# Kernel tuning notes

Hardware: AMD Instinct MI355X
Metric: run time of the kernel (lower is better)

The kernel has to match this reference:

```python
import jax, jax.numpy as jnp
import numpy as np

N_NODES = 100_000
N_EDGES = 600_000
D = 128  # in_channels


def setup_inputs() -> dict:
    key = jax.random.key(0)
    k1, k2, k3, k4, k5 = jax.random.split(key, 5)
    node_embs_src = jax.random.normal(k1, (N_NODES, D), dtype=jnp.float32)
    node_embs_dst = jax.random.normal(k2, (N_NODES, D), dtype=jnp.float32)
    edge_index = jax.random.randint(k3, (2, N_EDGES), 0, N_NODES, dtype=jnp.int64)
    # MLP params: Linear(2D -> D), Linear(D -> 1); scaled like default torch init
    W1 = jax.random.normal(k4, (2 * D, D), dtype=jnp.float32) / np.sqrt(2 * D)
    b1 = jnp.zeros((D,), dtype=jnp.float32)
    W2 = jax.random.normal(k5, (D, 1), dtype=jnp.float32) / np.sqrt(D)
    b2 = jnp.zeros((1,), dtype=jnp.float32)
    return {
        "node_embs_src": node_embs_src,
        "node_embs_dst": node_embs_dst,
        "edge_index": edge_index,
        "W1": W1,
        "b1": b1,
        "W2": W2,
        "b2": b2,
    }


def reference(node_embs_src, node_embs_dst, edge_index, W1, b1, W2, b2):
    # Gather per-edge source / destination embeddings: [E, D] each
    src = node_embs_src[edge_index[0]]
    dst = node_embs_dst[edge_index[1]]
    # concat([src, dst]) @ W1 == src @ W1[:D] + dst @ W1[D:]  (avoids materializing [E, 2D])
    h = jnp.dot(src, W1[:D]) + jnp.dot(dst, W1[D:]) + b1  # [E, D]
    h = jax.nn.relu(h)
    logits = jnp.dot(h, W2) + b2  # [E, 1]
    return jax.nn.sigmoid(logits)
```

## Files before the change

kernel.cpp:

```cpp
#include <hip/hip_runtime.h>
#include <stdint.h>

typedef __attribute__((ext_vector_type(8))) short short8;
typedef __attribute__((ext_vector_type(4))) float f32x4;

__device__ __forceinline__ unsigned short f2bf(float f) {
  union { float f; uint32_t u; } v; v.f = f;
  uint32_t u = v.u;
  uint32_t r = (u + 0x7FFFu + ((u >> 16) & 1u)) >> 16;
  return (unsigned short)r;
}
__device__ __forceinline__ float bf2f(unsigned short h) {
  union { uint32_t u; float f; } v; v.u = ((uint32_t)h) << 16; return v.f;
}

#define NBM 64
__global__ __launch_bounds__(256, 8)
void node_phase_kernel(const float* __restrict__ src_emb,
                       const float* __restrict__ dst_emb,
                       const float* __restrict__ W1,
                       unsigned short* __restrict__ UV,
                       int Nn, int ntiles) {
  __shared__ __align__(16) char Als[NBM * 256];

  const int tbl = blockIdx.y;
  const float* emb = tbl ? dst_emb : src_emb;
  const float* Wt  = W1 + (size_t)tbl * 128 * 128;
  unsigned short* outp = UV + (size_t)tbl * Nn * 128;

  const int tid  = threadIdx.x;
  const int lane = tid & 63;
  const int w    = tid >> 6;
  const int l15  = lane & 15;
  const int lk8  = (lane >> 4) * 8;

  short8 bfrag[4][2];
#pragma unroll
  for (int s = 0; s < 4; ++s) {
#pragma unroll
    for (int nf = 0; nf < 2; ++nf) {
      const int col = w * 32 + nf * 16 + l15;
      short8 t;
#pragma unroll
      for (int j = 0; j < 8; ++j) {
        const int k = s * 32 + lk8 + j;
        t[j] = (short)f2bf(Wt[k * 128 + col]);
      }
      bfrag[s][nf] = t;
    }
  }

  const int q = tid & 15, r0 = tid >> 4;
  const int swz = (l15 & 7) << 4;

  for (int t = blockIdx.x; t < ntiles; t += gridDim.x) {
    const int t0 = t * NBM;

#pragma unroll
    for (int i = 0; i < 4; ++i) {
      const int row = i * 16 + r0;
      const int node = t0 + row;
      if (node < Nn) {
        const float* base = emb + (size_t)node * 128 + q * 8;
        const float4 f0 = *(const float4*)base;
        const float4 f1 = *(const float4*)(base + 4);
        short8 hv;
        hv[0] = (short)f2bf(f0.x); hv[1] = (short)f2bf(f0.y);
        hv[2] = (short)f2bf(f0.z); hv[3] = (short)f2bf(f0.w);
        hv[4] = (short)f2bf(f1.x); hv[5] = (short)f2bf(f1.y);
        hv[6] = (short)f2bf(f1.z); hv[7] = (short)f2bf(f1.w);
        const int byteoff = row * 256 + ((q * 16) ^ ((row & 7) << 4));
        *(short8*)(Als + byteoff) = hv;
      }
    }
    __syncthreads();

#pragma unroll
    for (int m = 0; m < 4; ++m) {
      f32x4 acc0 = {0.f, 0.f, 0.f, 0.f};
      f32x4 acc1 = {0.f, 0.f, 0.f, 0.f};
      const int rowb = (m * 16 + l15) * 256;
      const int kb0  = lk8 * 2;
#pragma unroll
      for (int s = 0; s < 4; ++s) {
        const int off = rowb + ((s * 64 + kb0) ^ swz);
        const short8 a = *(const short8*)(Als + off);
        acc0 = __builtin_amdgcn_mfma_f32_16x16x32_bf16(a, bfrag[s][0], acc0, 0, 0, 0);
        acc1 = __builtin_amdgcn_mfma_f32_16x16x32_bf16(a, bfrag[s][1], acc1, 0, 0, 0);
      }
#pragma unroll
      for (int reg = 0; reg < 4; ++reg) {
        const int orow = t0 + m * 16 + ((lane >> 4) * 4) + reg;
        if (orow < Nn) {
          outp[(size_t)orow * 128 + w * 32 + l15]      = f2bf(acc0[reg]);
          outp[(size_t)orow * 128 + w * 32 + 16 + l15] = f2bf(acc1[reg]);
        }
      }
    }
    __syncthreads();
  }
}

__global__ __launch_bounds__(256, 8)
void edge_phase_kernel(const unsigned short* __restrict__ UV,
                       const int* __restrict__ eidx,
                       const float* __restrict__ b1,
                       const float* __restrict__ W2,
                       const float* __restrict__ b2,
                       float* __restrict__ out,
                       int E, int Nn) {
  const int tid = threadIdx.x;
  const int l15 = tid & 15;
  const int sg  = tid >> 4;

  float b1s[8], w2s[8];
#pragma unroll
  for (int j = 0; j < 8; ++j) {
    b1s[j] = b1[l15 * 8 + j];
    w2s[j] = W2[l15 * 8 + j];
  }
  const float b2s = b2[0];
  const unsigned short* U = UV;
  const unsigned short* V = UV + (size_t)Nn * 128;
  const int stride = gridDim.x * 16;

#pragma unroll 2
  for (int e = blockIdx.x * 16 + sg; e < E; e += stride) {
    const int s = eidx[e];
    const int d = eidx[E + e];
    const short8 u8 = *(const short8*)(U + (size_t)s * 128 + l15 * 8);
    const short8 v8 = *(const short8*)(V + (size_t)d * 128 + l15 * 8);
    float acc = 0.f;
#pragma unroll
    for (int j = 0; j < 8; ++j) {
      float g = bf2f((unsigned short)u8[j]) + bf2f((unsigned short)v8[j]) + b1s[j];
      g = g > 0.f ? g : 0.f;
      acc = fmaf(g, w2s[j], acc);
    }
#pragma unroll
    for (int off = 1; off < 16; off <<= 1)
      acc += __shfl_xor(acc, off, 64);
    if (l15 == 0) out[e] = 1.f / (1.f + __expf(-acc));
  }
}

#define BM 64
__global__ __launch_bounds__(256, 4)
void edge_decoder_fused(const float* __restrict__ src_emb,
                        const float* __restrict__ dst_emb,
                        const int* __restrict__ eidx,
                        const float* __restrict__ W1,
                        const float* __restrict__ b1,
                        const float* __restrict__ W2,
                        const float* __restrict__ b2,
                        float* __restrict__ out,
                        int E, int ntiles) {
  __shared__ __align__(16) char Als[BM * 512];
  __shared__ float rowpart[4][BM];

  const int tid  = threadIdx.x;
  const int lane = tid & 63;
  const int w    = tid >> 6;
  const int l15  = lane & 15;
  const int lk8  = (lane >> 4) * 8;

  short8 bfrag[8][2];
#pragma unroll
  for (int s = 0; s < 8; ++s) {
#pragma unroll
    for (int nf = 0; nf < 2; ++nf) {
      const int col = w * 32 + nf * 16 + l15;
      short8 t;
#pragma unroll
      for (int j = 0; j < 8; ++j) {
        const int k = s * 32 + lk8 + j;
        t[j] = (short)f2bf(W1[k * 128 + col]);
      }
      bfrag[s][nf] = t;
    }
  }
  float b1v[2], w2v[2];
#pragma unroll
  for (int nf = 0; nf < 2; ++nf) {
    const int col = w * 32 + nf * 16 + l15;
    b1v[nf] = b1[col];
    w2v[nf] = W2[col];
  }
  const float b2s = b2[0];

  const int q  = tid & 31;
  const int r0 = tid >> 5;
  const int qq = q & 15;
  const bool is_src = (q < 16);
  const int swz = (l15 & 7) << 4;

  for (int t = blockIdx.x; t < ntiles; t += gridDim.x) {
    const int t0 = t * BM;
#pragma unroll
    for (int i = 0; i < 8; ++i) {
      const int row = i * 8 + r0;
      const int e = t0 + row;
      if (e < E) {
        const int node = is_src ? eidx[e] : eidx[E + e];
        const float* base = (is_src ? src_emb : dst_emb) + (size_t)node * 128 + qq * 8;
        const float4 f0 = *(const float4*)base;
        const float4 f1 = *(const float4*)(base + 4);
        short8 hv;
        hv[0] = (short)f2bf(f0.x); hv[1] = (short)f2bf(f0.y);
        hv[2] = (short)f2bf(f0.z); hv[3] = (short)f2bf(f0.w);
        hv[4] = (short)f2bf(f1.x); hv[5] = (short)f2bf(f1.y);
        hv[6] = (short)f2bf(f1.z); hv[7] = (short)f2bf(f1.w);
        const int byteoff = row * 512 + ((q * 16) ^ ((row & 7) << 4));
        *(short8*)(Als + byteoff) = hv;
      }
    }
    __syncthreads();

    for (int m = 0; m < 4; ++m) {
      f32x4 acc0 = {0.f, 0.f, 0.f, 0.f};
      f32x4 acc1 = {0.f, 0.f, 0.f, 0.f};
      const int rowb = (m * 16 + l15) * 512;
      const int kb0  = lk8 * 2;
#pragma unroll
      for (int s = 0; s < 8; ++s) {
        const int off = rowb + ((s * 64 + kb0) ^ swz);
        const short8 a = *(const short8*)(Als + off);
        acc0 = __builtin_amdgcn_mfma_f32_16x16x32_bf16(a, bfrag[s][0], acc0, 0, 0, 0);
        acc1 = __builtin_amdgcn_mfma_f32_16x16x32_bf16(a, bfrag[s][1], acc1, 0, 0, 0);
      }
      float pr[4];
#pragma unroll
      for (int reg = 0; reg < 4; ++reg) {
        float h0 = acc0[reg] + b1v[0]; h0 = h0 > 0.f ? h0 : 0.f;
        float h1 = acc1[reg] + b1v[1]; h1 = h1 > 0.f ? h1 : 0.f;
        pr[reg] = h0 * w2v[0] + h1 * w2v[1];
      }
#pragma unroll
      for (int off = 1; off < 16; off <<= 1) {
#pragma unroll
        for (int reg = 0; reg < 4; ++reg)
          pr[reg] += __shfl_xor(pr[reg], off, 64);
      }
      if (l15 == 0) {
        const int rbase = m * 16 + (lane >> 4) * 4;
#pragma unroll
        for (int reg = 0; reg < 4; ++reg)
          rowpart[w][rbase + reg] = pr[reg];
      }
    }
    __syncthreads();

    if (tid < BM) {
      const int e = t0 + tid;
      if (e < E) {
        const float sum = rowpart[0][tid] + rowpart[1][tid] +
                          rowpart[2][tid] + rowpart[3][tid] + b2s;
        out[e] = 1.f / (1.f + __expf(-sum));
      }
    }
    __syncthreads();
  }
}

extern "C" void kernel_launch(void* const* d_in, const int* in_sizes, int n_in,
                              void* d_out, int out_size, void* d_ws, size_t ws_size,
                              hipStream_t stream) {
  const float* src = (const float*)d_in[0];
  const float* dst = (const float*)d_in[1];
  const int*   eix = (const int*)d_in[2];
  const float* W1  = (const float*)d_in[3];
  const float* b1  = (const float*)d_in[4];
  const float* W2  = (const float*)d_in[5];
  const float* b2  = (const float*)d_in[6];
  float* out = (float*)d_out;

  const int E  = in_sizes[2] / 2;
  const int Nn = in_sizes[0] / 128;
  const size_t uv_bytes = (size_t)Nn * 128 * 2 * sizeof(unsigned short);

  if (ws_size >= uv_bytes) {
    unsigned short* UV = (unsigned short*)d_ws;
    const int ntiles_n = (Nn + NBM - 1) / NBM;
    const int gx = ntiles_n < 512 ? ntiles_n : 512;
    node_phase_kernel<<<dim3(gx, 2), 256, 0, stream>>>(src, dst, W1, UV, Nn, ntiles_n);
    const int nblk = ((E + 15) / 16 < 2048) ? (E + 15) / 16 : 2048;
    edge_phase_kernel<<<nblk, 256, 0, stream>>>(UV, eix, b1, W2, b2, out, E, Nn);
  } else {
    const int ntiles = (E + BM - 1) / BM;
    const int grid = ntiles < 2048 ? ntiles : 2048;
    edge_decoder_fused<<<grid, 256, 0, stream>>>(src, dst, eix, W1, b1, W2, b2,
                                                 out, E, ntiles);
  }
}
```

Before: 75.68 us.

## Prefetch next node tile into registers and pack bf16 output stores

The node-phase kernel now loads the next tile's fp32 embeddings into registers while the current tile's MFMAs run, so global-load latency overlaps with compute. B-fragment columns are interleaved so each lane owns two adjacent output columns, which lets the two bf16 results go out as one 32-bit store instead of two 16-bit stores. The launch-bounds occupancy hint drops from 8 to 4 to make room for the extra prefetch registers, which may cost some latency hiding from fewer resident waves.

```diff
diff --git a/kernel.cpp b/kernel.cpp
--- a/kernel.cpp
+++ b/kernel.cpp
@@ -15,7 +15,7 @@
 }
 
 #define NBM 64
-__global__ __launch_bounds__(256, 8)
+__global__ __launch_bounds__(256, 4)
 void node_phase_kernel(const float* __restrict__ src_emb,
                        const float* __restrict__ dst_emb,
                        const float* __restrict__ W1,
@@ -39,7 +39,7 @@
   for (int s = 0; s < 4; ++s) {
 #pragma unroll
     for (int nf = 0; nf < 2; ++nf) {
-      const int col = w * 32 + nf * 16 + l15;
+      const int col = w * 32 + 2 * l15 + nf;
       short8 t;
 #pragma unroll
       for (int j = 0; j < 8; ++j) {
@@ -52,28 +52,47 @@
 
   const int q = tid & 15, r0 = tid >> 4;
   const int swz = (l15 & 7) << 4;
-
-  for (int t = blockIdx.x; t < ntiles; t += gridDim.x) {
+  const int gx = gridDim.x;
+
+  float4 p0[4], p1[4];
+#pragma unroll
+  for (int i = 0; i < 4; ++i) {
+    const int node = blockIdx.x * NBM + i * 16 + r0;
+    if (node < Nn) {
+      const float* base = emb + (size_t)node * 128 + q * 8;
+      p0[i] = *(const float4*)base;
+      p1[i] = *(const float4*)(base + 4);
+    }
+  }
+
+  for (int t = blockIdx.x; t < ntiles; t += gx) {
     const int t0 = t * NBM;
 
 #pragma unroll
     for (int i = 0; i < 4; ++i) {
       const int row = i * 16 + r0;
-      const int node = t0 + row;
-      if (node < Nn) {
-        const float* base = emb + (size_t)node * 128 + q * 8;
-        const float4 f0 = *(const float4*)base;
-        const float4 f1 = *(const float4*)(base + 4);
-        short8 hv;
-        hv[0] = (short)f2bf(f0.x); hv[1] = (short)f2bf(f0.y);
-        hv[2] = (short)f2bf(f0.z); hv[3] = (short)f2bf(f0.w);
-        hv[4] = (short)f2bf(f1.x); hv[5] = (short)f2bf(f1.y);
-        hv[6] = (short)f2bf(f1.z); hv[7] = (short)f2bf(f1.w);
-        const int byteoff = row * 256 + ((q * 16) ^ ((row & 7) << 4));
-        *(short8*)(Als + byteoff) = hv;
-      }
-    }
-    __syncthreads();
+      short8 hv;
+      hv[0] = (short)f2bf(p0[i].x); hv[1] = (short)f2bf(p0[i].y);
+      hv[2] = (short)f2bf(p0[i].z); hv[3] = (short)f2bf(p0[i].w);
+      hv[4] = (short)f2bf(p1[i].x); hv[5] = (short)f2bf(p1[i].y);
+      hv[6] = (short)f2bf(p1[i].z); hv[7] = (short)f2bf(p1[i].w);
+      const int byteoff = row * 256 + ((q * 16) ^ ((row & 7) << 4));
+      *(short8*)(Als + byteoff) = hv;
+    }
+    __syncthreads();
+
+    const int tn = t + gx;
+    if (tn < ntiles) {
+#pragma unroll
+      for (int i = 0; i < 4; ++i) {
+        const int node = tn * NBM + i * 16 + r0;
+        if (node < Nn) {
+          const float* base = emb + (size_t)node * 128 + q * 8;
+          p0[i] = *(const float4*)base;
+          p1[i] = *(const float4*)(base + 4);
+        }
+      }
+    }
 
 #pragma unroll
     for (int m = 0; m < 4; ++m) {
@@ -88,12 +107,14 @@
         acc0 = __builtin_amdgcn_mfma_f32_16x16x32_bf16(a, bfrag[s][0], acc0, 0, 0, 0);
         acc1 = __builtin_amdgcn_mfma_f32_16x16x32_bf16(a, bfrag[s][1], acc1, 0, 0, 0);
       }
+      const int col0 = w * 32 + 2 * l15;
 #pragma unroll
       for (int reg = 0; reg < 4; ++reg) {
         const int orow = t0 + m * 16 + ((lane >> 4) * 4) + reg;
         if (orow < Nn) {
-          outp[(size_t)orow * 128 + w * 32 + l15]      = f2bf(acc0[reg]);
-          outp[(size_t)orow * 128 + w * 32 + 16 + l15] = f2bf(acc1[reg]);
+          const uint32_t pk = (uint32_t)f2bf(acc0[reg]) |
+                              ((uint32_t)f2bf(acc1[reg]) << 16);
+          *(uint32_t*)&outp[(size_t)orow * 128 + col0] = pk;
         }
       }
     }
```

Result: no change. 76.02 us (+0.4%).
